# Performance work log

Measured on AMD Instinct MI355X. Metric: run time of the kernel, lower is better.

Reference implementation:

```python
import jax, jax.numpy as jnp
import numpy as np

M, N_ATOMS, N_BONDS, MAX_NB = 96, 96, 96, 3
HB = 158        # bond hidden size; linear is 2*HB -> HB
F_ATOM = 133    # unused by forward, present in signature


def _glorot(key, shape):
    fan_in = shape[1]
    return (jax.random.normal(key, shape, jnp.float32) / np.float32(np.sqrt(fan_in)))


def setup_inputs() -> dict:
    key = jax.random.key(0)
    ks = jax.random.split(key, 12)
    return {
        "a2b_": jax.random.randint(ks[0], (M, N_ATOMS, MAX_NB), 1, N_BONDS + 1, dtype=jnp.int32),
        "b2a_": jax.random.randint(ks[1], (M, N_BONDS), 0, N_ATOMS, dtype=jnp.int32),
        "b2revb_": jax.random.randint(ks[2], (M, N_BONDS), 0, N_BONDS, dtype=jnp.int32),
        "f_bonds_": jax.random.normal(ks[3], (M, N_BONDS, HB), jnp.float32),
        "f_atoms_": jax.random.normal(ks[4], (M, N_ATOMS, F_ATOM), jnp.float32),
        "bond_sum_": jnp.zeros((M, HB), jnp.float32),
        "W0": _glorot(ks[5], (HB, 2 * HB)), "b0": jnp.zeros((HB,), jnp.float32),
        "W1": _glorot(ks[6], (110, HB)),    "b1": jnp.zeros((110,), jnp.float32),
        "W2": _glorot(ks[7], (70, 110)),    "b2": jnp.zeros((70,), jnp.float32),
        "W3": _glorot(ks[8], (35, 70)),     "b3": jnp.zeros((35,), jnp.float32),
        "W4": _glorot(ks[9], (1, 35)),      "b4": jnp.zeros((1,), jnp.float32),
    }


def _message_pass(f_bonds, bond_sum, a2b, b2a, b2revb, W0, b0):
    # Faithful sequential replay of the nested python loops for one molecule.
    # f_bonds[c] is overwritten inside the inner loop (torch row view aliases),
    # and bond_sum carries across both loops -> single scan over (c, j) pairs.
    cs = jnp.repeat(jnp.arange(N_BONDS), MAX_NB)
    js = jnp.tile(jnp.arange(MAX_NB), N_BONDS)

    def step(carry, cj):
        fb, bs = carry
        c, j = cj
        d = a2b[b2a[c], j]                      # neighbor bond index (>=1 by construction)
        bs = fb[d - 1] + bs
        bs = bs - fb[b2revb[c]]
        nf = jnp.concatenate([fb[c], bs]) @ W0.T + b0   # 316 -> 158
        fb = fb.at[c].set(nf)
        return (fb, bs), None

    (fb, _), _ = jax.lax.scan(step, (f_bonds, bond_sum), (cs, js))
    return fb.sum(axis=0)                       # [HB]


def reference(a2b_, b2a_, b2revb_, f_bonds_, f_atoms_, bond_sum_,
              W0, b0, W1, b1, W2, b2, W3, b3, W4, b4):
    # f_atoms_ is accepted but never used, exactly as in the source module.
    mp = jax.vmap(_message_pass, in_axes=(0, 0, 0, 0, 0, None, None))(
        f_bonds_, bond_sum_, a2b_, b2a_, b2revb_, W0, b0)   # [M, HB]
    # Dropout layers are identity in eval mode. No activation after layer1 (per source).
    h = mp @ W1.T + b1
    h = jax.nn.relu(h @ W2.T + b2)
    h = jax.nn.relu(h @ W3.T + b3)
    out = h @ W4.T + b4                                    # [M, 1]
    return out.reshape(-1)                                 # cat of [1]-tensors -> [M]
```

## Files before the change

kernel.cpp:

```cpp
#include <hip/hip_runtime.h>

#define NBOND 96
#define HBS 158
#define NSTEP 288
#define NT 320

__global__ __launch_bounds__(NT, 1)
void gcn_mp_kernel(const int* __restrict__ a2b,
                   const int* __restrict__ b2a,
                   const int* __restrict__ b2revb,
                   const float* __restrict__ f_bonds,
                   const float* __restrict__ bond_sum,
                   const float* __restrict__ W0,
                   const float* __restrict__ b0,
                   const float* __restrict__ W1, const float* __restrict__ b1,
                   const float* __restrict__ W2, const float* __restrict__ b2v,
                   const float* __restrict__ W3, const float* __restrict__ b3,
                   const float* __restrict__ W4, const float* __restrict__ b4,
                   float* __restrict__ out)
{
  const int m  = blockIdx.x;
  const int t  = threadIdx.x;
  const int og = t >> 3;
  const int s  = t & 7;

  __shared__ __align__(16) float fb[NBOND * 160];
  __shared__ __align__(16) float xv[2][320];
  __shared__ int sDp[NSTEP];
  __shared__ int sRp[NSTEP];
  __shared__ __align__(16) float mpb[160];
  __shared__ float hb1[112], hb2[72], hb3[40];

  for (int idx = t; idx < NBOND * 160; idx += NT) {
    int r = idx / 160, o = idx - r * 160;
    fb[idx] = (o < HBS) ? f_bonds[(m * NBOND + r) * HBS + o] : 0.f;
  }
  if (t < NSTEP) {
    int i = t, c = i / 3, j = i - 3 * c;
    int a  = b2a[m * NBOND + c];
    int d  = a2b[(m * NBOND + a) * 3 + j] - 1;
    int rv = b2revb[m * NBOND + c];
    int cp = (i == 0) ? -1 : (i - 1) / 3;
    sDp[i] = d  | ((d  == cp) ? 0x10000 : 0);
    sRp[i] = rv | ((rv == cp) ? 0x10000 : 0);
  }

  float w[4][40];
  float b0r[4];
#pragma unroll
  for (int r = 0; r < 4; ++r) {
    const int o = og * 4 + r;
    b0r[r] = (o < HBS) ? b0[o] : 0.f;
#pragma unroll
    for (int kk = 0; kk < 40; ++kk) {
      const int k = s * 40 + kk;
      const int col = (k < 160) ? k : (k - 2);
      const bool valid = (o < HBS) && ((k < 160) ? (k < HBS) : (k < 160 + HBS));
      w[r][kk] = valid ? W0[o * (2 * HBS) + col] : 0.f;
    }
  }
  __syncthreads();

  if (t < 160) {
    int d0 = sDp[0] & 0xFFFF, r0 = sRp[0] & 0xFFFF;
    xv[0][t] = fb[t];
    float bsv = ((t < HBS) ? bond_sum[m * HBS + t] : 0.f)
              + fb[d0 * 160 + t] - fb[r0 * 160 + t];
    xv[0][160 + t] = bsv;
  }
  __syncthreads();

  float cs0 = 0.f, cs1 = 0.f, cs2 = 0.f, cs3 = 0.f;
  int p = 0;

#pragma unroll 1
  for (int i = 0; i < NSTEP; ++i) {
    const int c  = i / 3;
    const int j  = i - 3 * c;
    const int i1 = i + 1;
    const int c1 = i1 / 3;
    const int j1 = i1 - 3 * c1;
    const bool hn = (i1 < NSTEP);

    const float4* xp = (const float4*)(&xv[p][s * 40]);
    float4 x0 = xp[0], x1 = xp[1], x2 = xp[2], x3 = xp[3], x4 = xp[4];
    float4 x5 = xp[5], x6 = xp[6], x7 = xp[7], x8 = xp[8], x9 = xp[9];

    float4 nxr = make_float4(0.f, 0.f, 0.f, 0.f);
    float2 dd = make_float2(0.f, 0.f), rr = make_float2(0.f, 0.f), bo = make_float2(0.f, 0.f);
    int aD = 0, aR = 0, e0 = 0;
    if (hn) {
      if (s == 1 && j1 == 0) {
        nxr = *(const float4*)(&fb[c1 * 160 + og * 4]);
      }
      if (s >= 2 && s <= 3) {
        const int pd = sDp[i1], pr = sRp[i1];
        const int d  = pd & 0xFFFF;  aD = pd >> 16;
        const int rv = pr & 0xFFFF;  aR = pr >> 16;
        e0 = og * 4 + (s - 2) * 2;
        dd = *(const float2*)(&fb[d  * 160 + e0]);
        rr = *(const float2*)(&fb[rv * 160 + e0]);
        bo = *(const float2*)(&xv[p][160 + e0]);
      }
    }

    float a0 = 0.f, a1 = 0.f, a2 = 0.f, a3 = 0.f;
#define QSTEP(qq, xx) \
    a0 = fmaf(w[0][4*qq+0], xx.x, a0); a1 = fmaf(w[1][4*qq+0], xx.x, a1); \
    a2 = fmaf(w[2][4*qq+0], xx.x, a2); a3 = fmaf(w[3][4*qq+0], xx.x, a3); \
    a0 = fmaf(w[0][4*qq+1], xx.y, a0); a1 = fmaf(w[1][4*qq+1], xx.y, a1); \
    a2 = fmaf(w[2][4*qq+1], xx.y, a2); a3 = fmaf(w[3][4*qq+1], xx.y, a3); \
    a0 = fmaf(w[0][4*qq+2], xx.z, a0); a1 = fmaf(w[1][4*qq+2], xx.z, a1); \
    a2 = fmaf(w[2][4*qq+2], xx.z, a2); a3 = fmaf(w[3][4*qq+2], xx.z, a3); \
    a0 = fmaf(w[0][4*qq+3], xx.w, a0); a1 = fmaf(w[1][4*qq+3], xx.w, a1); \
    a2 = fmaf(w[2][4*qq+3], xx.w, a2); a3 = fmaf(w[3][4*qq+3], xx.w, a3);
    QSTEP(0, x0) QSTEP(1, x1) QSTEP(2, x2) QSTEP(3, x3) QSTEP(4, x4)
    QSTEP(5, x5) QSTEP(6, x6) QSTEP(7, x7) QSTEP(8, x8) QSTEP(9, x9)
#undef QSTEP

    a0 += __shfl_xor(a0, 1); a0 += __shfl_xor(a0, 2); a0 += __shfl_xor(a0, 4);
    a1 += __shfl_xor(a1, 1); a1 += __shfl_xor(a1, 2); a1 += __shfl_xor(a1, 4);
    a2 += __shfl_xor(a2, 1); a2 += __shfl_xor(a2, 2); a2 += __shfl_xor(a2, 4);
    a3 += __shfl_xor(a3, 1); a3 += __shfl_xor(a3, 2); a3 += __shfl_xor(a3, 4);
    a0 += b0r[0]; a1 += b0r[1]; a2 += b0r[2]; a3 += b0r[3];

    if (s == 0) {
      *(float4*)(&fb[c * 160 + og * 4]) = make_float4(a0, a1, a2, a3);
    }
    if (hn) {
      if (s == 1) {
        float4 wv = (j1 == 0) ? nxr : make_float4(a0, a1, a2, a3);
        *(float4*)(&xv[p ^ 1][og * 4]) = wv;
      }
      if (s >= 2 && s <= 3) {
        float sA = (s == 2) ? a0 : a2;
        float sB = (s == 2) ? a1 : a3;
        float vd0 = aD ? sA : dd.x;
        float vd1 = aD ? sB : dd.y;
        float vr0 = aR ? sA : rr.x;
        float vr1 = aR ? sB : rr.y;
        *(float2*)(&xv[p ^ 1][160 + e0]) =
            make_float2(bo.x + vd0 - vr0, bo.y + vd1 - vr1);
      }
    }
    if (j == 2) { cs0 += a0; cs1 += a1; cs2 += a2; cs3 += a3; }

    p ^= 1;
    __syncthreads();
  }

  if (s == 0) {
    *(float4*)(&mpb[og * 4]) = make_float4(cs0, cs1, cs2, cs3);
  }
  __syncthreads();

  if (t < 110) {
    float acc = b1[t];
    for (int k = 0; k < HBS; ++k) acc = fmaf(mpb[k], W1[t * HBS + k], acc);
    hb1[t] = acc;
  }
  __syncthreads();
  if (t < 70) {
    float acc = b2v[t];
    for (int k = 0; k < 110; ++k) acc = fmaf(hb1[k], W2[t * 110 + k], acc);
    hb2[t] = fmaxf(acc, 0.f);
  }
  __syncthreads();
  if (t < 35) {
    float acc = b3[t];
    for (int k = 0; k < 70; ++k) acc = fmaf(hb2[k], W3[t * 70 + k], acc);
    hb3[t] = fmaxf(acc, 0.f);
  }
  __syncthreads();
  if (t == 0) {
    float acc = b4[0];
    for (int k = 0; k < 35; ++k) acc = fmaf(hb3[k], W4[k], acc);
    out[m] = acc;
  }
}

extern "C" void kernel_launch(void* const* d_in, const int* in_sizes, int n_in,
                              void* d_out, int out_size, void* d_ws, size_t ws_size,
                              hipStream_t stream)
{
  const int*   a2b      = (const int*)d_in[0];
  const int*   b2a      = (const int*)d_in[1];
  const int*   b2revb   = (const int*)d_in[2];
  const float* f_bonds  = (const float*)d_in[3];
  const float* bond_sum = (const float*)d_in[5];
  const float* W0 = (const float*)d_in[6];
  const float* b0 = (const float*)d_in[7];
  const float* W1 = (const float*)d_in[8];
  const float* b1 = (const float*)d_in[9];
  const float* W2 = (const float*)d_in[10];
  const float* b2 = (const float*)d_in[11];
  const float* W3 = (const float*)d_in[12];
  const float* b3 = (const float*)d_in[13];
  const float* W4 = (const float*)d_in[14];
  const float* b4 = (const float*)d_in[15];

  gcn_mp_kernel<<<dim3(96), dim3(NT), 0, stream>>>(
      a2b, b2a, b2revb, f_bonds, bond_sum,
      W0, b0, W1, b1, W2, b2, W3, b3, W4, b4,
      (float*)d_out);
}
```

Measured before the change: 302.5 us.

## Split matvec across ten waves with LDS weight staging and cross-wave reduction

Doubles the block to 640 threads and splits the 316-wide input dimension across ten wavefronts, each owning a 32-column slice. Part of W0 is staged in LDS, the rest is reloaded from global/L2 every step, and partial sums are reduced through shared memory with an extra barrier per step. When the workspace is large enough, the f_bonds state moves to a global workspace so LDS can hold more weights. The aim is more parallelism per sequential step. The cost is an extra __syncthreads per step, repeated global weight loads, and a serial 10-way reduction done by 160 threads.

```diff
diff --git a/kernel.cpp b/kernel.cpp
--- a/kernel.cpp
+++ b/kernel.cpp
@@ -1,10 +1,21 @@
 #include <hip/hip_runtime.h>
 
 #define NBOND 96
-#define HBS 158
+#define HBS   158
 #define NSTEP 288
-#define NT 320
-
+#define NT    640
+#define NW    10
+#define WCOLS 316
+
+typedef float f4 __attribute__((ext_vector_type(4)));
+
+__device__ __forceinline__ f4 ld4(const float* p) {
+  float2 lo = *(const float2*)(p);
+  float2 hi = *(const float2*)(p + 2);
+  return (f4){lo.x, lo.y, hi.x, hi.y};
+}
+
+template<bool FBG>
 __global__ __launch_bounds__(NT, 1)
 void gcn_mp_kernel(const int* __restrict__ a2b,
                    const int* __restrict__ b2a,
@@ -17,24 +28,36 @@
                    const float* __restrict__ W2, const float* __restrict__ b2v,
                    const float* __restrict__ W3, const float* __restrict__ b3,
                    const float* __restrict__ W4, const float* __restrict__ b4,
-                   float* __restrict__ out)
+                   float* __restrict__ out,
+                   float* __restrict__ fbws)
 {
+  constexpr int LW4 = FBG ? 14 : 8;
+  constexpr int NA  = FBG ? 2  : 8;
+
   const int m  = blockIdx.x;
   const int t  = threadIdx.x;
-  const int og = t >> 3;
-  const int s  = t & 7;
-
-  __shared__ __align__(16) float fb[NBOND * 160];
+  const int w  = t >> 6;
+  const int og = t & 63;
+
+  __shared__ __align__(16) f4 Wld[LW4 * NT];
   __shared__ __align__(16) float xv[2][320];
-  __shared__ int sDp[NSTEP];
-  __shared__ int sRp[NSTEP];
-  __shared__ __align__(16) float mpb[160];
+  __shared__ float part[NW * 160];
+  __shared__ int   sDp[NSTEP], sRp[NSTEP];
+  __shared__ float mpb[160];
   __shared__ float hb1[112], hb2[72], hb3[40];
-
-  for (int idx = t; idx < NBOND * 160; idx += NT) {
-    int r = idx / 160, o = idx - r * 160;
-    fb[idx] = (o < HBS) ? f_bonds[(m * NBOND + r) * HBS + o] : 0.f;
-  }
+  __shared__ float fbl[FBG ? 1 : NBOND * HBS];
+
+  float* const fbg = fbws + (size_t)m * (NBOND * HBS);
+  auto FBld = [&](int idx) -> float {
+    if constexpr (FBG) return fbg[idx]; else return fbl[idx];
+  };
+  auto FBst = [&](int idx, float v) {
+    if constexpr (FBG) fbg[idx] = v; else fbl[idx] = v;
+  };
+
+  for (int idx = t; idx < NBOND * HBS; idx += NT)
+    FBst(idx, f_bonds[m * (NBOND * HBS) + idx]);
+
   if (t < NSTEP) {
     int i = t, c = i / 3, j = i - 3 * c;
     int a  = b2a[m * NBOND + c];
@@ -45,32 +68,45 @@
     sRp[i] = rv | ((rv == cp) ? 0x10000 : 0);
   }
 
-  float w[4][40];
-  float b0r[4];
-#pragma unroll
-  for (int r = 0; r < 4; ++r) {
-    const int o = og * 4 + r;
-    b0r[r] = (o < HBS) ? b0[o] : 0.f;
-#pragma unroll
-    for (int kk = 0; kk < 40; ++kk) {
-      const int k = s * 40 + kk;
-      const int col = (k < 160) ? k : (k - 2);
-      const bool valid = (o < HBS) && ((k < 160) ? (k < HBS) : (k < 160 + HBS));
-      w[r][kk] = valid ? W0[o * (2 * HBS) + col] : 0.f;
-    }
-  }
+  const int kb    = w * 32;
+  const int cbase = kb - (kb >= 160 ? 2 : 0);
+
+#pragma unroll
+  for (int sid = 0; sid < LW4; ++sid) {
+    const int a = sid >> 3, q = sid & 7;
+    const int o = og + 64 * a;
+    Wld[sid * NT + t] = ld4(W0 + o * WCOLS + cbase + q * 4);
+  }
+  const float* LpA[NA];
+#pragma unroll
+  for (int u = 0; u < NA; ++u) {
+    const int q = 8 - NA + u;
+    LpA[u] = W0 + (og + 64) * WCOLS + cbase + q * 4;
+  }
+  const bool hasB = (og < 32);
+  int oB = og + 128; if (oB > 157) oB = 157;
+  const float* LpB[8];
+#pragma unroll
+  for (int q = 0; q < 8; ++q)
+    LpB[q] = W0 + oB * WCOLS + cbase + q * 4;
+
+  const float b0v = (t < HBS) ? b0[t] : 0.f;
+
   __syncthreads();
 
   if (t < 160) {
-    int d0 = sDp[0] & 0xFFFF, r0 = sRp[0] & 0xFFFF;
-    xv[0][t] = fb[t];
-    float bsv = ((t < HBS) ? bond_sum[m * HBS + t] : 0.f)
-              + fb[d0 * 160 + t] - fb[r0 * 160 + t];
-    xv[0][160 + t] = bsv;
-  }
-  __syncthreads();
-
-  float cs0 = 0.f, cs1 = 0.f, cs2 = 0.f, cs3 = 0.f;
+    float x0 = 0.f, bs0 = 0.f;
+    if (t < HBS) {
+      int d0 = sDp[0] & 0xFFFF, r0 = sRp[0] & 0xFFFF;
+      x0  = FBld(t);
+      bs0 = bond_sum[m * HBS + t] + FBld(d0 * HBS + t) - FBld(r0 * HBS + t);
+    }
+    xv[0][t]       = x0;
+    xv[0][160 + t] = bs0;
+  }
+  __syncthreads();
+
+  float cs = 0.f;
   int p = 0;
 
 #pragma unroll 1
@@ -82,76 +118,95 @@
     const int j1 = i1 - 3 * c1;
     const bool hn = (i1 < NSTEP);
 
-    const float4* xp = (const float4*)(&xv[p][s * 40]);
-    float4 x0 = xp[0], x1 = xp[1], x2 = xp[2], x3 = xp[3], x4 = xp[4];
-    float4 x5 = xp[5], x6 = xp[6], x7 = xp[7], x8 = xp[8], x9 = xp[9];
-
-    float4 nxr = make_float4(0.f, 0.f, 0.f, 0.f);
-    float2 dd = make_float2(0.f, 0.f), rr = make_float2(0.f, 0.f), bo = make_float2(0.f, 0.f);
-    int aD = 0, aR = 0, e0 = 0;
-    if (hn) {
-      if (s == 1 && j1 == 0) {
-        nxr = *(const float4*)(&fb[c1 * 160 + og * 4]);
-      }
-      if (s >= 2 && s <= 3) {
-        const int pd = sDp[i1], pr = sRp[i1];
-        const int d  = pd & 0xFFFF;  aD = pd >> 16;
-        const int rv = pr & 0xFFFF;  aR = pr >> 16;
-        e0 = og * 4 + (s - 2) * 2;
-        dd = *(const float2*)(&fb[d  * 160 + e0]);
-        rr = *(const float2*)(&fb[rv * 160 + e0]);
-        bo = *(const float2*)(&xv[p][160 + e0]);
-      }
-    }
-
-    float a0 = 0.f, a1 = 0.f, a2 = 0.f, a3 = 0.f;
-#define QSTEP(qq, xx) \
-    a0 = fmaf(w[0][4*qq+0], xx.x, a0); a1 = fmaf(w[1][4*qq+0], xx.x, a1); \
-    a2 = fmaf(w[2][4*qq+0], xx.x, a2); a3 = fmaf(w[3][4*qq+0], xx.x, a3); \
-    a0 = fmaf(w[0][4*qq+1], xx.y, a0); a1 = fmaf(w[1][4*qq+1], xx.y, a1); \
-    a2 = fmaf(w[2][4*qq+1], xx.y, a2); a3 = fmaf(w[3][4*qq+1], xx.y, a3); \
-    a0 = fmaf(w[0][4*qq+2], xx.z, a0); a1 = fmaf(w[1][4*qq+2], xx.z, a1); \
-    a2 = fmaf(w[2][4*qq+2], xx.z, a2); a3 = fmaf(w[3][4*qq+2], xx.z, a3); \
-    a0 = fmaf(w[0][4*qq+3], xx.w, a0); a1 = fmaf(w[1][4*qq+3], xx.w, a1); \
-    a2 = fmaf(w[2][4*qq+3], xx.w, a2); a3 = fmaf(w[3][4*qq+3], xx.w, a3);
-    QSTEP(0, x0) QSTEP(1, x1) QSTEP(2, x2) QSTEP(3, x3) QSTEP(4, x4)
-    QSTEP(5, x5) QSTEP(6, x6) QSTEP(7, x7) QSTEP(8, x8) QSTEP(9, x9)
-#undef QSTEP
-
-    a0 += __shfl_xor(a0, 1); a0 += __shfl_xor(a0, 2); a0 += __shfl_xor(a0, 4);
-    a1 += __shfl_xor(a1, 1); a1 += __shfl_xor(a1, 2); a1 += __shfl_xor(a1, 4);
-    a2 += __shfl_xor(a2, 1); a2 += __shfl_xor(a2, 2); a2 += __shfl_xor(a2, 4);
-    a3 += __shfl_xor(a3, 1); a3 += __shfl_xor(a3, 2); a3 += __shfl_xor(a3, 4);
-    a0 += b0r[0]; a1 += b0r[1]; a2 += b0r[2]; a3 += b0r[3];
-
-    if (s == 0) {
-      *(float4*)(&fb[c * 160 + og * 4]) = make_float4(a0, a1, a2, a3);
-    }
-    if (hn) {
-      if (s == 1) {
-        float4 wv = (j1 == 0) ? nxr : make_float4(a0, a1, a2, a3);
-        *(float4*)(&xv[p ^ 1][og * 4]) = wv;
-      }
-      if (s >= 2 && s <= 3) {
-        float sA = (s == 2) ? a0 : a2;
-        float sB = (s == 2) ? a1 : a3;
-        float vd0 = aD ? sA : dd.x;
-        float vd1 = aD ? sB : dd.y;
-        float vr0 = aR ? sA : rr.x;
-        float vr1 = aR ? sB : rr.y;
-        *(float2*)(&xv[p ^ 1][160 + e0]) =
-            make_float2(bo.x + vd0 - vr0, bo.y + vd1 - vr1);
-      }
-    }
-    if (j == 2) { cs0 += a0; cs1 += a1; cs2 += a2; cs3 += a3; }
-
+    f4 xq[8];
+    const f4* XP = (const f4*)(&xv[p][w * 32]);
+#pragma unroll
+    for (int q = 0; q < 8; ++q) xq[q] = XP[q];
+
+    f4 wa[NA];
+#pragma unroll
+    for (int u = 0; u < NA; ++u) wa[u] = ld4(LpA[u]);
+    f4 wb[8];
+    if (hasB) {
+#pragma unroll
+      for (int q = 0; q < 8; ++q) wb[q] = ld4(LpB[q]);
+    }
+
+    float dd = 0.f, rr = 0.f, bo = 0.f, prx = 0.f;
+    int aD = 0, aR = 0;
+    if (t < 160 && hn) {
+      const int pd = sDp[i1], pr = sRp[i1];
+      const int d  = pd & 0xFFFF;  aD = pd >> 16;
+      const int rv = pr & 0xFFFF;  aR = pr >> 16;
+      bo = xv[p][160 + t];
+      if (t < HBS) {
+        dd = FBld(d * HBS + t);
+        rr = FBld(rv * HBS + t);
+        if (j1 == 0) prx = FBld(c1 * HBS + t);
+      }
+    }
+
+    float a0 = 0.f, a1 = 0.f, a2s = 0.f;
+#pragma unroll
+    for (int q = 0; q < 8; ++q) {
+      const f4 v = Wld[q * NT + t];
+      a0 = fmaf(v[0], xq[q][0], a0); a0 = fmaf(v[1], xq[q][1], a0);
+      a0 = fmaf(v[2], xq[q][2], a0); a0 = fmaf(v[3], xq[q][3], a0);
+    }
+    if constexpr (FBG) {
+#pragma unroll
+      for (int q = 0; q < 6; ++q) {
+        const f4 v = Wld[(8 + q) * NT + t];
+        a1 = fmaf(v[0], xq[q][0], a1); a1 = fmaf(v[1], xq[q][1], a1);
+        a1 = fmaf(v[2], xq[q][2], a1); a1 = fmaf(v[3], xq[q][3], a1);
+      }
+#pragma unroll
+      for (int u = 0; u < 2; ++u) {
+        const f4 v = wa[u];
+        a1 = fmaf(v[0], xq[6 + u][0], a1); a1 = fmaf(v[1], xq[6 + u][1], a1);
+        a1 = fmaf(v[2], xq[6 + u][2], a1); a1 = fmaf(v[3], xq[6 + u][3], a1);
+      }
+    } else {
+#pragma unroll
+      for (int q = 0; q < 8; ++q) {
+        const f4 v = wa[q];
+        a1 = fmaf(v[0], xq[q][0], a1); a1 = fmaf(v[1], xq[q][1], a1);
+        a1 = fmaf(v[2], xq[q][2], a1); a1 = fmaf(v[3], xq[q][3], a1);
+      }
+    }
+    if (hasB) {
+#pragma unroll
+      for (int q = 0; q < 8; ++q) {
+        const f4 v = wb[q];
+        a2s = fmaf(v[0], xq[q][0], a2s); a2s = fmaf(v[1], xq[q][1], a2s);
+        a2s = fmaf(v[2], xq[q][2], a2s); a2s = fmaf(v[3], xq[q][3], a2s);
+      }
+    }
+
+    part[w * 160 + og]      = a0;
+    part[w * 160 + og + 64] = a1;
+    if (hasB) part[w * 160 + og + 128] = a2s;
+    __syncthreads();
+
+    if (t < 160) {
+      float nf = b0v;
+#pragma unroll
+      for (int u = 0; u < NW; ++u) nf += part[u * 160 + t];
+      if (t < HBS) FBst(c * HBS + t, nf);
+      if (j == 2) cs += nf;
+      if (hn) {
+        float xnew = (j1 == 0) ? prx : nf;
+        float bsn  = bo + (aD ? nf : dd) - (aR ? nf : rr);
+        if (t >= HBS) { xnew = 0.f; bsn = 0.f; }
+        xv[p ^ 1][t]       = xnew;
+        xv[p ^ 1][160 + t] = bsn;
+      }
+    }
     p ^= 1;
     __syncthreads();
   }
 
-  if (s == 0) {
-    *(float4*)(&mpb[og * 4]) = make_float4(cs0, cs1, cs2, cs3);
-  }
+  if (t < 160) mpb[t] = (t < HBS) ? cs : 0.f;
   __syncthreads();
 
   if (t < 110) {
@@ -199,8 +254,16 @@
   const float* W4 = (const float*)d_in[14];
   const float* b4 = (const float*)d_in[15];
 
-  gcn_mp_kernel<<<dim3(96), dim3(NT), 0, stream>>>(
-      a2b, b2a, b2revb, f_bonds, bond_sum,
-      W0, b0, W1, b1, W2, b2, W3, b3, W4, b4,
-      (float*)d_out);
+  const size_t need = (size_t)96 * NBOND * HBS * sizeof(float);
+  if (ws_size >= need) {
+    gcn_mp_kernel<true><<<dim3(96), dim3(NT), 0, stream>>>(
+        a2b, b2a, b2revb, f_bonds, bond_sum,
+        W0, b0, W1, b1, W2, b2, W3, b3, W4, b4,
+        (float*)d_out, (float*)d_ws);
+  } else {
+    gcn_mp_kernel<false><<<dim3(96), dim3(NT), 0, stream>>>(
+        a2b, b2a, b2revb, f_bonds, bond_sum,
+        W0, b0, W1, b1, W2, b2, W3, b3, W4, b4,
+        (float*)d_out, (float*)d_ws);
+  }
 }
```

Result: slower. 404.1 us (+33.6%).
